# Kernel optimization log

Measured on AMD Instinct MI355X. Metric: run time of the kernel, lower is better.

Reference implementation:

```python
import jax, jax.numpy as jnp
import numpy as np

B, T, H, W, D, NH = 8, 16, 14, 14, 768, 12
HID = int(D * 4.0)
HEAD_DIM = D // NH
EPS = 1e-5


def _ln(x, w, b):
    m = x.mean(-1, keepdims=True)
    v = ((x - m) ** 2).mean(-1, keepdims=True)
    return (x - m) * jax.lax.rsqrt(v + EPS) * w + b


def _attn(x, qkv_w, proj_w, proj_b):
    # x: [Bn, S, D]; qkv_w: [D, 3D] (no bias); proj: [D, D] + bias
    Bn, S, _ = x.shape
    qkv = (x @ qkv_w).reshape(Bn, S, 3, NH, HEAD_DIM).transpose(2, 0, 3, 1, 4)
    q, k, v = qkv[0], qkv[1], qkv[2]
    a = jnp.einsum('bhqd,bhkd->bhqk', q, k) * (HEAD_DIM ** -0.5)
    a = jax.nn.softmax(a, axis=-1)
    o = jnp.einsum('bhqk,bhkd->bhqd', a, v).transpose(0, 2, 1, 3).reshape(Bn, S, D)
    return o @ proj_w + proj_b


def setup_inputs() -> dict:
    key = jax.random.key(0)
    ks = jax.random.split(key, 20)
    N = H * W * T
    s = 0.02
    f32 = jnp.float32
    return {
        'x': jax.random.normal(ks[0], (B, 1 + N, D), f32),
        'tn1_w': jnp.ones((D,), f32), 'tn1_b': jnp.zeros((D,), f32),
        't_qkv_w': jax.random.normal(ks[1], (D, 3 * D), f32) * s,
        't_proj_w': jax.random.normal(ks[2], (D, D), f32) * s,
        't_proj_b': jnp.zeros((D,), f32),
        'tfc_w': jax.random.normal(ks[3], (D, D), f32) * s,
        'tfc_b': jnp.zeros((D,), f32),
        'n1_w': jnp.ones((D,), f32), 'n1_b': jnp.zeros((D,), f32),
        's_qkv_w': jax.random.normal(ks[4], (D, 3 * D), f32) * s,
        's_proj_w': jax.random.normal(ks[5], (D, D), f32) * s,
        's_proj_b': jnp.zeros((D,), f32),
        'n2_w': jnp.ones((D,), f32), 'n2_b': jnp.zeros((D,), f32),
        'fc1_w': jax.random.normal(ks[6], (D, HID), f32) * s,
        'fc1_b': jnp.zeros((HID,), f32),
        'fc2_w': jax.random.normal(ks[7], (HID, D), f32) * s,
        'fc2_b': jnp.zeros((D,), f32),
        'pt_mask': jnp.ones((B, 1 + N), dtype=bool),
        't_frames': T, 'height': H, 'width': W,
    }


def reference(x, tn1_w, tn1_b, t_qkv_w, t_proj_w, t_proj_b, tfc_w, tfc_b,
              n1_w, n1_b, s_qkv_w, s_proj_w, s_proj_b, n2_w, n2_b,
              fc1_w, fc1_b, fc2_w, fc2_b, pt_mask, t_frames, height, width):
    # divided space-time attention; USE_CLS_TOKEN=True, use_pt_visibility=False
    b = x.shape[0]
    t, h, w = t_frames, height, width
    n = h * w * t
    # --- temporal attention over t per (b, h, w) ---
    xt = x[:, 1:, :].reshape(b * h * w, t, D)  # 'b (h w t) m -> (b h w) t m'
    rt = _attn(_ln(xt, tn1_w, tn1_b), t_qkv_w, t_proj_w, t_proj_b)
    rt = rt.reshape(b, n, D) @ tfc_w + tfc_b  # temporal_fc
    xt2 = x[:, 1:, :] + rt
    init_cls = x[:, 0:1, :]  # [b, 1, D]
    # --- spatial attention over (1 + h*w) per (b, t) ---
    cls_tok = jnp.broadcast_to(init_cls, (b, t, D)).reshape(b * t, 1, D)
    xs = xt2.reshape(b, h * w, t, D).transpose(0, 2, 1, 3).reshape(b * t, h * w, D)
    xs = jnp.concatenate([cls_tok, xs], axis=1)  # [(b t), 1+hw, D]
    rs = _attn(_ln(xs, n1_w, n1_b), s_qkv_w, s_proj_w, s_proj_b)
    cls_out = rs[:, 0, :].reshape(b, t, D).mean(axis=1, keepdims=True)
    rs = rs[:, 1:, :].reshape(b, t, h * w, D).transpose(0, 2, 1, 3).reshape(b, n, D)
    x_new = jnp.concatenate([init_cls, xt2], axis=1) + jnp.concatenate([cls_out, rs], axis=1)
    # --- MLP block ---
    y = _ln(x_new, n2_w, n2_b)
    y = jax.nn.gelu(y @ fc1_w + fc1_b, approximate=False) @ fc2_w + fc2_b
    return x_new + y
```

## Files before the change

### kernel.cpp

```cpp
#include <hip/hip_runtime.h>
#include <cstdint>

using u16 = unsigned short;
using u32 = unsigned int;

typedef __bf16 bf16x8 __attribute__((ext_vector_type(8)));
typedef float  floatx4 __attribute__((ext_vector_type(4)));

#define DEV static __device__ __forceinline__

DEV u16 f2bf(float f) {
    u32 u = __float_as_uint(f);
    u += 0x7FFFu + ((u >> 16) & 1u);
    return (u16)(u >> 16);
}
DEV float bf2f(u16 v) { return __uint_as_float(((u32)v) << 16); }

DEV floatx4 mfma32(bf16x8 a, bf16x8 b, floatx4 c) {
    return __builtin_amdgcn_mfma_f32_16x16x32_bf16(a, b, c, 0, 0, 0);
}

DEV floatx4 fzero() { floatx4 z; z[0]=0.f; z[1]=0.f; z[2]=0.f; z[3]=0.f; return z; }

__global__ __launch_bounds__(256) void transpose_w(
    const float* __restrict__ W, u16* __restrict__ Wt, int K, int N)
{
    __shared__ float t[32][33];
    const int tx = threadIdx.x, ty = threadIdx.y;
    const int gx = blockIdx.x * 32;
    const int gy = blockIdx.y * 32;
    #pragma unroll
    for (int i = 0; i < 4; ++i)
        t[ty + i*8][tx] = W[(size_t)(gy + ty + i*8) * N + gx + tx];
    __syncthreads();
    #pragma unroll
    for (int i = 0; i < 4; ++i)
        Wt[(size_t)(gx + ty + i*8) * K + gy + tx] = f2bf(t[tx][ty + i*8]);
}

template<int MODE>
__global__ __launch_bounds__(256) void ln_kernel(
    const float* __restrict__ xp, const u16* __restrict__ xt2,
    const float* __restrict__ w, const float* __restrict__ b,
    u16* __restrict__ out, int nrows)
{
    const int row = blockIdx.x * 4 + (threadIdx.x >> 6);
    if (row >= nrows) return;
    const int lane = threadIdx.x & 63;
    float vals[12];
    if constexpr (MODE == 0) {
        const float* src = xp + (size_t)(row + row/3136 + 1) * 768;
        #pragma unroll
        for (int j = 0; j < 3; ++j) {
            float4 v = reinterpret_cast<const float4*>(src)[j*64 + lane];
            vals[j*4+0]=v.x; vals[j*4+1]=v.y; vals[j*4+2]=v.z; vals[j*4+3]=v.w;
        }
    } else {
        const int bt = row / 197;
        const int p  = row - bt * 197;
        const int b0 = bt >> 4, tt = bt & 15;
        if (p == 0) {
            const float* src = xp + (size_t)b0 * 3137 * 768;
            #pragma unroll
            for (int j = 0; j < 3; ++j) {
                float4 v = reinterpret_cast<const float4*>(src)[j*64 + lane];
                vals[j*4+0]=v.x; vals[j*4+1]=v.y; vals[j*4+2]=v.z; vals[j*4+3]=v.w;
            }
        } else {
            const u16* src = xt2 + (size_t)(b0*3136 + (p-1)*16 + tt) * 768;
            #pragma unroll
            for (int j = 0; j < 3; ++j) {
                uint2 q = reinterpret_cast<const uint2*>(src)[j*64 + lane];
                vals[j*4+0] = bf2f((u16)(q.x & 0xFFFF));
                vals[j*4+1] = bf2f((u16)(q.x >> 16));
                vals[j*4+2] = bf2f((u16)(q.y & 0xFFFF));
                vals[j*4+3] = bf2f((u16)(q.y >> 16));
            }
        }
    }
    float s = 0.f, ss = 0.f;
    #pragma unroll
    for (int e = 0; e < 12; ++e) { s += vals[e]; ss += vals[e]*vals[e]; }
    #pragma unroll
    for (int o = 32; o > 0; o >>= 1) { s += __shfl_xor(s, o); ss += __shfl_xor(ss, o); }
    const float mean = s * (1.f/768.f);
    const float var  = ss * (1.f/768.f) - mean*mean;
    const float rstd = rsqrtf(var + 1e-5f);
    #pragma unroll
    for (int j = 0; j < 3; ++j) {
        const int c4 = (j*64 + lane) * 4;
        union { u16 u[4]; uint2 q; } o;
        #pragma unroll
        for (int e = 0; e < 4; ++e)
            o.u[e] = f2bf((vals[j*4+e] - mean)*rstd*w[c4+e] + b[c4+e]);
        *reinterpret_cast<uint2*>(&out[(size_t)row*768 + c4]) = o.q;
    }
}

__global__ __launch_bounds__(256) void combine_ln2(
    const float* __restrict__ xp, const u16* __restrict__ xt2,
    const u16* __restrict__ rsb, const float* __restrict__ w, const float* __restrict__ b,
    float* __restrict__ xnew, u16* __restrict__ ln2, int nrows)
{
    const int row = blockIdx.x * 4 + (threadIdx.x >> 6);
    if (row >= nrows) return;
    const int lane = threadIdx.x & 63;
    const int b0 = row / 3137;
    const int j  = row - b0 * 3137;
    float vals[12];
    if (j == 0) {
        #pragma unroll
        for (int e = 0; e < 12; ++e) {
            const int c = e*64 + lane;
            float acc = 0.f;
            for (int t = 0; t < 16; ++t)
                acc += bf2f(rsb[(size_t)(b0*16 + t) * 197 * 768 + c]);
            vals[e] = xp[(size_t)row*768 + c] + acc * (1.f/16.f);
        }
    } else {
        const int n_idx = j - 1;
        const int hw = n_idx >> 4, tt = n_idx & 15;
        const u16* a  = xt2 + (size_t)(b0*3136 + n_idx) * 768;
        const u16* r2 = rsb + (size_t)((b0*16 + tt)*197 + 1 + hw) * 768;
        #pragma unroll
        for (int e = 0; e < 12; ++e) {
            const int c = e*64 + lane;
            vals[e] = bf2f(a[c]) + bf2f(r2[c]);
        }
    }
    float s = 0.f, ss = 0.f;
    #pragma unroll
    for (int e = 0; e < 12; ++e) { s += vals[e]; ss += vals[e]*vals[e]; }
    #pragma unroll
    for (int o = 32; o > 0; o >>= 1) { s += __shfl_xor(s, o); ss += __shfl_xor(ss, o); }
    const float mean = s * (1.f/768.f);
    const float var  = ss * (1.f/768.f) - mean*mean;
    const float rstd = rsqrtf(var + 1e-5f);
    #pragma unroll
    for (int e = 0; e < 12; ++e) {
        const int c = e*64 + lane;
        xnew[(size_t)row*768 + c] = vals[e];
        ln2[(size_t)row*768 + c]  = f2bf((vals[e] - mean)*rstd*w[c] + b[c]);
    }
}

template<int RESID, bool BIAS, bool GELU_ACT, bool OUTF, bool OUTB, bool MASKM>
__global__ __launch_bounds__(256) void gemm_bt(
    const u16* __restrict__ A, const u16* __restrict__ Bt,
    const float* __restrict__ bias, const float* __restrict__ resid,
    float* __restrict__ Cf, u16* __restrict__ Cb,
    int N, int K, int lda, int ldb, int Mvalid)
{
    __shared__ __attribute__((aligned(16))) u16 As[128*32];
    __shared__ __attribute__((aligned(16))) u16 Bs[128*32];
    const int tid  = threadIdx.x;
    const int wave = tid >> 6;
    const int lane = tid & 63;
    const int m15  = lane & 15;
    const int quad = lane >> 4;
    const int wm = wave >> 1, wn = wave & 1;
    const long m0 = (long)blockIdx.x * 128;
    const long n0 = (long)blockIdx.y * 128;

    const int c0 = wave*128 + lane;
    const int c1 = wave*128 + 64 + lane;
    const u16* Ag0 = A  + (size_t)(m0 + (c0 >> 2)) * lda + (c0 & 3) * 8;
    const u16* Ag1 = A  + (size_t)(m0 + (c1 >> 2)) * lda + (c1 & 3) * 8;
    const u16* Bg0 = Bt + (size_t)(n0 + (c0 >> 2)) * ldb + (c0 & 3) * 8;
    const u16* Bg1 = Bt + (size_t)(n0 + (c1 >> 2)) * ldb + (c1 & 3) * 8;
    u16* Al0 = &As[(size_t)c0 * 8];
    u16* Al1 = &As[(size_t)c1 * 8];
    u16* Bl0 = &Bs[(size_t)c0 * 8];
    u16* Bl1 = &Bs[(size_t)c1 * 8];

    floatx4 acc[4][4];
    #pragma unroll
    for (int i = 0; i < 4; ++i)
        #pragma unroll
        for (int j = 0; j < 4; ++j) acc[i][j] = fzero();

    for (int k0 = 0; k0 < K; k0 += 32) {
        const uint4 ra0 = *reinterpret_cast<const uint4*>(Ag0 + k0);
        const uint4 ra1 = *reinterpret_cast<const uint4*>(Ag1 + k0);
        const uint4 rb0 = *reinterpret_cast<const uint4*>(Bg0 + k0);
        const uint4 rb1 = *reinterpret_cast<const uint4*>(Bg1 + k0);
        __syncthreads();
        *reinterpret_cast<uint4*>(Al0) = ra0;
        *reinterpret_cast<uint4*>(Al1) = ra1;
        *reinterpret_cast<uint4*>(Bl0) = rb0;
        *reinterpret_cast<uint4*>(Bl1) = rb1;
        __syncthreads();
        bf16x8 af[4], bf[4];
        #pragma unroll
        for (int i = 0; i < 4; ++i)
            af[i] = *reinterpret_cast<const bf16x8*>(&As[(wm*64 + i*16 + m15)*32 + quad*8]);
        #pragma unroll
        for (int j = 0; j < 4; ++j)
            bf[j] = *reinterpret_cast<const bf16x8*>(&Bs[(wn*64 + j*16 + m15)*32 + quad*8]);
        #pragma unroll
        for (int i = 0; i < 4; ++i)
            #pragma unroll
            for (int j = 0; j < 4; ++j)
                acc[i][j] = mfma32(af[i], bf[j], acc[i][j]);
    }

    #pragma unroll
    for (int j = 0; j < 4; ++j) {
        const long col = n0 + wn*64 + j*16 + m15;
        float bv = 0.f;
        if constexpr (BIAS) bv = bias[col];
        #pragma unroll
        for (int i = 0; i < 4; ++i) {
            const long rowb = m0 + wm*64 + i*16 + quad*4;
            #pragma unroll
            for (int r = 0; r < 4; ++r) {
                const long row = rowb + r;
                if constexpr (MASKM) { if (row >= Mvalid) continue; }
                float v = acc[i][j][r] + bv;
                if constexpr (RESID == 1) v += resid[(size_t)row * N + col];
                if constexpr (RESID == 2) v += resid[(size_t)(row + row/3136 + 1) * 768 + col];
                if constexpr (GELU_ACT)   v = 0.5f * v * (1.f + erff(v * 0.70710678118f));
                if constexpr (OUTF) Cf[(size_t)row * N + col] = v;
                if constexpr (OUTB) Cb[(size_t)row * N + col] = f2bf(v);
            }
        }
    }
}

template<int S, int NQ, int NIT>
__global__ __launch_bounds__(256) void attn_kernel(
    const u16* __restrict__ qkv, u16* __restrict__ out, int ntask)
{
    __shared__ __attribute__((aligned(16))) u16 P_lds[4][16*32];
    const int wave = threadIdx.x >> 6;
    const int lane = threadIdx.x & 63;
    const int task = blockIdx.x * 4 + wave;
    if (task >= ntask) return;
    const int seq  = task / (12 * NQ);
    const int rem  = task - seq * (12 * NQ);
    const int head = rem / NQ;
    const int qt   = rem - head * NQ;
    const int m15  = lane & 15;
    const int quad = lane >> 4;
    const size_t base = (size_t)seq * S;

    const u16* qp = qkv + (base + qt*16 + m15) * 2304 + head*64 + quad*8;
    const bf16x8 Qf0 = *reinterpret_cast<const bf16x8*>(qp);
    const bf16x8 Qf1 = *reinterpret_cast<const bf16x8*>(qp + 32);

    floatx4 Oacc[4];
    #pragma unroll
    for (int c = 0; c < 4; ++c) Oacc[c] = fzero();
    float mrun = -__builtin_inff();
    float lrun = 0.f;
    u16* P = &P_lds[wave][0];

    for (int it = 0; it < NIT; ++it) {
        const int j0 = it * 32;
        floatx4 st[2];
        #pragma unroll
        for (int h2 = 0; h2 < 2; ++h2) {
            const u16* kp = qkv + (base + j0 + h2*16 + m15) * 2304 + 768 + head*64 + quad*8;
            const bf16x8 K0 = *reinterpret_cast<const bf16x8*>(kp);
            const bf16x8 K1 = *reinterpret_cast<const bf16x8*>(kp + 32);
            floatx4 z = fzero();
            z = mfma32(K0, Qf0, z);
            st[h2] = mfma32(K1, Qf1, z);
        }
        float sc[8];
        #pragma unroll
        for (int h2 = 0; h2 < 2; ++h2)
            #pragma unroll
            for (int r = 0; r < 4; ++r) {
                const int jj = j0 + h2*16 + quad*4 + r;
                sc[h2*4+r] = (jj < S) ? st[h2][r] * 0.125f : -__builtin_inff();
            }
        float tmax = sc[0];
        #pragma unroll
        for (int k = 1; k < 8; ++k) tmax = fmaxf(tmax, sc[k]);
        tmax = fmaxf(tmax, __shfl_xor(tmax, 16));
        tmax = fmaxf(tmax, __shfl_xor(tmax, 32));
        const float mnew = fmaxf(mrun, tmax);
        float p[8], tsum = 0.f;
        #pragma unroll
        for (int k = 0; k < 8; ++k) { p[k] = __expf(sc[k] - mnew); tsum += p[k]; }
        tsum += __shfl_xor(tsum, 16);
        tsum += __shfl_xor(tsum, 32);
        const float alpha = __expf(mrun - mnew);
        lrun = lrun * alpha + tsum;
        mrun = mnew;
        #pragma unroll
        for (int r = 0; r < 4; ++r) {
            const float ar = __shfl(alpha, quad*4 + r);
            #pragma unroll
            for (int c = 0; c < 4; ++c) Oacc[c][r] *= ar;
        }
        #pragma unroll
        for (int h2 = 0; h2 < 2; ++h2)
            #pragma unroll
            for (int r = 0; r < 4; ++r)
                P[m15*32 + h2*16 + quad*4 + r] = f2bf(p[h2*4+r]);
        const bf16x8 Pf = *reinterpret_cast<const bf16x8*>(&P[m15*32 + quad*8]);
        #pragma unroll
        for (int c = 0; c < 4; ++c) {
            union { u16 u[8]; bf16x8 v; } vf;
            #pragma unroll
            for (int jj2 = 0; jj2 < 8; ++jj2)
                vf.u[jj2] = qkv[(base + j0 + quad*8 + jj2) * 2304 + 1536 + head*64 + c*16 + m15];
            Oacc[c] = mfma32(Pf, vf.v, Oacc[c]);
        }
    }
    const float linv_self = 1.f / lrun;
    #pragma unroll
    for (int r = 0; r < 4; ++r) {
        const int prow = qt*16 + quad*4 + r;
        const float linv = __shfl(linv_self, quad*4 + r);
        if (prow < S) {
            u16* op = out + (base + prow) * 768 + head*64 + m15;
            #pragma unroll
            for (int c = 0; c < 4; ++c) op[c*16] = f2bf(Oacc[c][r] * linv);
        }
    }
}

extern "C" void kernel_launch(void* const* d_in, const int* in_sizes, int n_in,
                              void* d_out, int out_size, void* d_ws, size_t ws_size,
                              hipStream_t stream)
{
    (void)in_sizes; (void)n_in; (void)out_size; (void)ws_size;
    const float* x        = (const float*)d_in[0];
    const float* tn1_w    = (const float*)d_in[1];
    const float* tn1_b    = (const float*)d_in[2];
    const float* t_qkv_w  = (const float*)d_in[3];
    const float* t_proj_w = (const float*)d_in[4];
    const float* t_proj_b = (const float*)d_in[5];
    const float* tfc_w    = (const float*)d_in[6];
    const float* tfc_b    = (const float*)d_in[7];
    const float* n1_w     = (const float*)d_in[8];
    const float* n1_b     = (const float*)d_in[9];
    const float* s_qkv_w  = (const float*)d_in[10];
    const float* s_proj_w = (const float*)d_in[11];
    const float* s_proj_b = (const float*)d_in[12];
    const float* n2_w     = (const float*)d_in[13];
    const float* n2_b     = (const float*)d_in[14];
    const float* fc1_w    = (const float*)d_in[15];
    const float* fc1_b    = (const float*)d_in[16];
    const float* fc2_w    = (const float*)d_in[17];
    const float* fc2_b    = (const float*)d_in[18];
    float* out = (float*)d_out;

    char* ws = (char*)d_ws;
    size_t off = 0;
    auto alloc = [&](size_t bytes) -> void* {
        void* p = ws + off;
        off += (bytes + 255) & ~(size_t)255;
        return p;
    };
    u16* wt_tqkv  = (u16*)alloc((size_t)768*2304*2);
    u16* wt_tproj = (u16*)alloc((size_t)768*768*2);
    u16* wt_tfc   = (u16*)alloc((size_t)768*768*2);
    u16* wt_sqkv  = (u16*)alloc((size_t)768*2304*2);
    u16* wt_sproj = (u16*)alloc((size_t)768*768*2);
    u16* wt_fc1   = (u16*)alloc((size_t)768*3072*2);
    u16* wt_fc2   = (u16*)alloc((size_t)3072*768*2);
    u16* slotA = (u16*)alloc((size_t)25280*2304*2);
    u16* slotB = (u16*)alloc((size_t)25216*768*2);
    u16* slotD = (u16*)alloc((size_t)25216*768*2);
    u16* slotE = (u16*)alloc((size_t)25216*768*2);

    dim3 tb(32, 8);
    transpose_w<<<dim3(72, 24), tb, 0, stream>>>(t_qkv_w,  wt_tqkv,  768, 2304);
    transpose_w<<<dim3(24, 24), tb, 0, stream>>>(t_proj_w, wt_tproj, 768, 768);
    transpose_w<<<dim3(24, 24), tb, 0, stream>>>(tfc_w,    wt_tfc,   768, 768);
    transpose_w<<<dim3(72, 24), tb, 0, stream>>>(s_qkv_w,  wt_sqkv,  768, 2304);
    transpose_w<<<dim3(24, 24), tb, 0, stream>>>(s_proj_w, wt_sproj, 768, 768);
    transpose_w<<<dim3(96, 24), tb, 0, stream>>>(fc1_w,    wt_fc1,   768, 3072);
    transpose_w<<<dim3(24, 96), tb, 0, stream>>>(fc2_w,    wt_fc2,   3072, 768);

    u16* lnT  = slotD;
    u16* qkvT = slotA;
    ln_kernel<0><<<25088/4, 256, 0, stream>>>(x, nullptr, tn1_w, tn1_b, lnT, 25088);
    gemm_bt<0,false,false,false,true,false><<<dim3(196,18), 256, 0, stream>>>(
        lnT, wt_tqkv, nullptr, nullptr, nullptr, qkvT, 2304, 768, 768, 768, 0);

    u16* attnT = slotD;
    attn_kernel<16,1,1><<<18816/4, 256, 0, stream>>>(qkvT, attnT, 18816);

    u16* hp = slotE;
    gemm_bt<0,true,false,false,true,false><<<dim3(196,6), 256, 0, stream>>>(
        attnT, wt_tproj, t_proj_b, nullptr, nullptr, hp, 768, 768, 768, 768, 0);

    u16* xt2 = slotB;
    gemm_bt<2,true,false,false,true,false><<<dim3(196,6), 256, 0, stream>>>(
        hp, wt_tfc, tfc_b, x, nullptr, xt2, 768, 768, 768, 768, 0);

    u16* lnS = slotD;
    ln_kernel<1><<<25216/4, 256, 0, stream>>>(x, xt2, n1_w, n1_b, lnS, 25216);

    u16* qkvS = slotA;
    gemm_bt<0,false,false,false,true,false><<<dim3(197,18), 256, 0, stream>>>(
        lnS, wt_sqkv, nullptr, nullptr, nullptr, qkvS, 2304, 768, 768, 768, 0);

    u16* attnS = slotD;
    attn_kernel<197,13,7><<<19968/4, 256, 0, stream>>>(qkvS, attnS, 19968);

    u16* rsb = slotE;
    gemm_bt<0,true,false,false,true,false><<<dim3(197,6), 256, 0, stream>>>(
        attnS, wt_sproj, s_proj_b, nullptr, nullptr, rsb, 768, 768, 768, 768, 0);

    float* xnew = out;
    u16* ln2 = slotD;
    combine_ln2<<<25096/4, 256, 0, stream>>>(x, xt2, rsb, n2_w, n2_b, xnew, ln2, 25096);

    u16* h1 = slotA;
    for (int half = 0; half < 2; ++half) {
        const u16* w1h = wt_fc1 + (size_t)half * 1536 * 768;
        const float* b1h = fc1_b + half * 1536;
        gemm_bt<0,true,true,false,true,false><<<dim3(197,12), 256, 0, stream>>>(
            ln2, w1h, b1h, nullptr, nullptr, h1, 1536, 768, 768, 768, 0);
        const u16* w2h = wt_fc2 + (size_t)half * 1536;
        if (half == 0)
            gemm_bt<1,true,false,true,false,true><<<dim3(197,6), 256, 0, stream>>>(
                h1, w2h, fc2_b, out, out, nullptr, 768, 1536, 1536, 3072, 25096);
        else
            gemm_bt<1,false,false,true,false,true><<<dim3(197,6), 256, 0, stream>>>(
                h1, w2h, nullptr, out, out, nullptr, 768, 1536, 1536, 3072, 25096);
    }
}
```

Baseline: 1.512 ms.

## Load GEMM tiles directly into LDS and swap grid axes for N-major order

The GEMM kernel now stages its A and B tiles with global_load_lds, which writes global data straight into LDS instead of going through registers. Each wave's LDS base is set per 64-lane chunk to match the hardware's per-lane placement. The grid is also transposed so blockIdx.x walks the N tiles, meaning consecutive blocks share the same A rows for better L2 reuse. The loop still uses two barriers and a single buffer, so load latency is not overlapped with compute, and correctness relies on the async load landing before the second barrier.

```diff
diff --git a/kernel.cpp b/kernel.cpp
--- a/kernel.cpp
+++ b/kernel.cpp
@@ -21,6 +21,14 @@
 }
 
 DEV floatx4 fzero() { floatx4 z; z[0]=0.f; z[1]=0.f; z[2]=0.f; z[3]=0.f; return z; }
+
+typedef __attribute__((address_space(3))) u32 as3_u32;
+typedef __attribute__((address_space(1))) u32 as1_u32;
+
+DEV void async_ld16(const u16* g, u16* l) {
+    __builtin_amdgcn_global_load_lds(
+        (const as1_u32*)g, (as3_u32*)l, 16, 0, 0);
+}
 
 __global__ __launch_bounds__(256) void transpose_w(
     const float* __restrict__ W, u16* __restrict__ Wt, int K, int N)
@@ -159,8 +167,8 @@
     const int m15  = lane & 15;
     const int quad = lane >> 4;
     const int wm = wave >> 1, wn = wave & 1;
-    const long m0 = (long)blockIdx.x * 128;
-    const long n0 = (long)blockIdx.y * 128;
+    const long m0 = (long)blockIdx.y * 128;
+    const long n0 = (long)blockIdx.x * 128;
 
     const int c0 = wave*128 + lane;
     const int c1 = wave*128 + 64 + lane;
@@ -168,10 +176,10 @@
     const u16* Ag1 = A  + (size_t)(m0 + (c1 >> 2)) * lda + (c1 & 3) * 8;
     const u16* Bg0 = Bt + (size_t)(n0 + (c0 >> 2)) * ldb + (c0 & 3) * 8;
     const u16* Bg1 = Bt + (size_t)(n0 + (c1 >> 2)) * ldb + (c1 & 3) * 8;
-    u16* Al0 = &As[(size_t)c0 * 8];
-    u16* Al1 = &As[(size_t)c1 * 8];
-    u16* Bl0 = &Bs[(size_t)c0 * 8];
-    u16* Bl1 = &Bs[(size_t)c1 * 8];
+    u16* Al0 = &As[(wave*2 + 0) * 512];
+    u16* Al1 = &As[(wave*2 + 1) * 512];
+    u16* Bl0 = &Bs[(wave*2 + 0) * 512];
+    u16* Bl1 = &Bs[(wave*2 + 1) * 512];
 
     floatx4 acc[4][4];
     #pragma unroll
@@ -180,15 +188,11 @@
         for (int j = 0; j < 4; ++j) acc[i][j] = fzero();
 
     for (int k0 = 0; k0 < K; k0 += 32) {
-        const uint4 ra0 = *reinterpret_cast<const uint4*>(Ag0 + k0);
-        const uint4 ra1 = *reinterpret_cast<const uint4*>(Ag1 + k0);
-        const uint4 rb0 = *reinterpret_cast<const uint4*>(Bg0 + k0);
-        const uint4 rb1 = *reinterpret_cast<const uint4*>(Bg1 + k0);
         __syncthreads();
-        *reinterpret_cast<uint4*>(Al0) = ra0;
-        *reinterpret_cast<uint4*>(Al1) = ra1;
-        *reinterpret_cast<uint4*>(Bl0) = rb0;
-        *reinterpret_cast<uint4*>(Bl1) = rb1;
+        async_ld16(Ag0 + k0, Al0);
+        async_ld16(Ag1 + k0, Al1);
+        async_ld16(Bg0 + k0, Bl0);
+        async_ld16(Bg1 + k0, Bl1);
         __syncthreads();
         bf16x8 af[4], bf[4];
         #pragma unroll
@@ -380,32 +384,32 @@
     u16* lnT  = slotD;
     u16* qkvT = slotA;
     ln_kernel<0><<<25088/4, 256, 0, stream>>>(x, nullptr, tn1_w, tn1_b, lnT, 25088);
-    gemm_bt<0,false,false,false,true,false><<<dim3(196,18), 256, 0, stream>>>(
+    gemm_bt<0,false,false,false,true,false><<<dim3(18,196), 256, 0, stream>>>(
         lnT, wt_tqkv, nullptr, nullptr, nullptr, qkvT, 2304, 768, 768, 768, 0);
 
     u16* attnT = slotD;
     attn_kernel<16,1,1><<<18816/4, 256, 0, stream>>>(qkvT, attnT, 18816);
 
     u16* hp = slotE;
-    gemm_bt<0,true,false,false,true,false><<<dim3(196,6), 256, 0, stream>>>(
+    gemm_bt<0,true,false,false,true,false><<<dim3(6,196), 256, 0, stream>>>(
         attnT, wt_tproj, t_proj_b, nullptr, nullptr, hp, 768, 768, 768, 768, 0);
 
     u16* xt2 = slotB;
-    gemm_bt<2,true,false,false,true,false><<<dim3(196,6), 256, 0, stream>>>(
+    gemm_bt<2,true,false,false,true,false><<<dim3(6,196), 256, 0, stream>>>(
         hp, wt_tfc, tfc_b, x, nullptr, xt2, 768, 768, 768, 768, 0);
 
     u16* lnS = slotD;
     ln_kernel<1><<<25216/4, 256, 0, stream>>>(x, xt2, n1_w, n1_b, lnS, 25216);
 
     u16* qkvS = slotA;
-    gemm_bt<0,false,false,false,true,false><<<dim3(197,18), 256, 0, stream>>>(
+    gemm_bt<0,false,false,false,true,false><<<dim3(18,197), 256, 0, stream>>>(
         lnS, wt_sqkv, nullptr, nullptr, nullptr, qkvS, 2304, 768, 768, 768, 0);
 
     u16* attnS = slotD;
     attn_kernel<197,13,7><<<19968/4, 256, 0, stream>>>(qkvS, attnS, 19968);
 
     u16* rsb = slotE;
-    gemm_bt<0,true,false,false,true,false><<<dim3(197,6), 256, 0, stream>>>(
+    gemm_bt<0,true,false,false,true,false><<<dim3(6,197), 256, 0, stream>>>(
         attnS, wt_sproj, s_proj_b, nullptr, nullptr, rsb, 768, 768, 768, 768, 0);
 
     float* xnew = out;
@@ -416,14 +420,14 @@
     for (int half = 0; half < 2; ++half) {
         const u16* w1h = wt_fc1 + (size_t)half * 1536 * 768;
         const float* b1h = fc1_b + half * 1536;
-        gemm_bt<0,true,true,false,true,false><<<dim3(197,12), 256, 0, stream>>>(
+        gemm_bt<0,true,true,false,true,false><<<dim3(12,197), 256, 0, stream>>>(
             ln2, w1h, b1h, nullptr, nullptr, h1, 1536, 768, 768, 768, 0);
         const u16* w2h = wt_fc2 + (size_t)half * 1536;
         if (half == 0)
-            gemm_bt<1,true,false,true,false,true><<<dim3(197,6), 256, 0, stream>>>(
+            gemm_bt<1,true,false,true,false,true><<<dim3(6,197), 256, 0, stream>>>(
                 h1, w2h, fc2_b, out, out, nullptr, 768, 1536, 1536, 3072, 25096);
         else
-            gemm_bt<1,false,false,true,false,true><<<dim3(197,6), 256, 0, stream>>>(
+            gemm_bt<1,false,false,true,false,true><<<dim3(6,197), 256, 0, stream>>>(
                 h1, w2h, nullptr, out, out, nullptr, 768, 1536, 1536, 3072, 25096);
     }
 }
```

After: 1.471 ms. 2.7% less time.
